# Kernel tuning notes

Hardware: AMD Instinct MI355X
Metric: run time of the kernel (lower is better)

Reference implementation:

```python
import jax, jax.numpy as jnp
import numpy as np

NU, NP, H = 100000, 200000, 128
EV, EL = 500000, 150000


def _sage(x_src, x_dst, src, dst, Wl, bl, Wr, n_dst):
    # PyG SAGEConv: lin_l(mean_j x_j) + lin_r(x_i); lin_l has bias, lin_r does not.
    msg = x_src[src]                                             # [E, H] gather
    agg = jax.ops.segment_sum(msg, dst, num_segments=n_dst)      # [n_dst, H]
    cnt = jax.ops.segment_sum(jnp.ones((src.shape[0],), x_src.dtype), dst,
                              num_segments=n_dst)                # [n_dst]
    mean = agg / jnp.maximum(cnt, 1.0)[:, None]
    return mean @ Wl.T + bl + x_dst @ Wr.T


def _hetero_layer(xu, xp, Wl, bl, Wr, ev_s, ev_d, el_s, el_d):
    # relation order: 0 viewed(u->p), 1 rev_viewed(p->u), 2 liked(u->p), 3 rev_liked(p->u)
    post = (_sage(xu, xp, ev_s, ev_d, Wl[0], bl[0], Wr[0], NP)
            + _sage(xu, xp, el_s, el_d, Wl[2], bl[2], Wr[2], NP))
    user = (_sage(xp, xu, ev_d, ev_s, Wl[1], bl[1], Wr[1], NU)
            + _sage(xp, xu, el_d, el_s, Wl[3], bl[3], Wr[3], NU))
    return user, post


def setup_inputs() -> dict:
    key = jax.random.key(0)
    ks = jax.random.split(key, 9)
    s = 1.0 / np.sqrt(H)
    return {
        "emb_user": jax.random.normal(ks[0], (NU, H), jnp.float32),
        "emb_post": jax.random.normal(ks[1], (NP, H), jnp.float32),
        "W_l": jax.random.normal(ks[2], (2, 4, H, H), jnp.float32) * s,
        "b_l": jnp.zeros((2, 4, H), jnp.float32),
        "W_r": jax.random.normal(ks[3], (2, 4, H, H), jnp.float32) * s,
        "viewed_src": jax.random.randint(ks[4], (EV,), 0, NU, jnp.int32),
        "viewed_dst": jax.random.randint(ks[5], (EV,), 0, NP, jnp.int32),
        "liked_src": jax.random.randint(ks[6], (EL,), 0, NU, jnp.int32),
        "liked_dst": jax.random.randint(ks[7], (EL,), 0, NP, jnp.int32),
    }


def reference(emb_user, emb_post, W_l, b_l, W_r,
              viewed_src, viewed_dst, liked_src, liked_dst):
    xu, xp = _hetero_layer(emb_user, emb_post, W_l[0], b_l[0], W_r[0],
                           viewed_src, viewed_dst, liked_src, liked_dst)
    xu, xp = jax.nn.relu(xu), jax.nn.relu(xp)
    xu, xp = _hetero_layer(xu, xp, W_l[1], b_l[1], W_r[1],
                           viewed_src, viewed_dst, liked_src, liked_dst)
    return xu, xp
```

## Files before the change

kernel.cpp:

```cpp
#include <hip/hip_runtime.h>
#include <hip/hip_bf16.h>

#define H 128

using bf16x8  = __attribute__((ext_vector_type(8))) short;
using floatx4 = __attribute__((ext_vector_type(4))) float;

static __device__ __forceinline__ short f2bf(float f) {
  union { float f; unsigned u; } v; v.f = f;
  unsigned r = v.u + 0x7fffu + ((v.u >> 16) & 1u);
  return (short)(r >> 16);
}
static __device__ __forceinline__ float bf2f(short s) {
  union { unsigned u; float f; } v; v.u = ((unsigned)(unsigned short)s) << 16;
  return v.f;
}

__global__ void count_edges2(const int* __restrict__ ev_s, const int* __restrict__ ev_d, int EV,
                             const int* __restrict__ el_s, const int* __restrict__ el_d, int EL,
                             int* __restrict__ cnt, int oV_u, int oV_p, int oL_u, int oL_p) {
  int i = blockIdx.x * blockDim.x + threadIdx.x;
  if (i < EV) {
    atomicAdd(&cnt[oV_u + ev_s[i]], 1);
    atomicAdd(&cnt[oV_p + ev_d[i]], 1);
  } else if (i - EV < EL) {
    int e = i - EV;
    atomicAdd(&cnt[oL_u + el_s[e]], 1);
    atomicAdd(&cnt[oL_p + el_d[e]], 1);
  }
}

__global__ __launch_bounds__(256) void scan_k1(const int* __restrict__ cnt, int* __restrict__ off,
                                               int* __restrict__ bsums, int4 starts, int4 lens) {
  int a = blockIdx.y;
  int start = ((const int*)&starts)[a];
  int len   = ((const int*)&lens)[a];
  int chunk = blockIdx.x * 1024;
  if (chunk >= len) return;
  const int* in = cnt + start;
  int* out = off + start;
  int tid = threadIdx.x;
  int base = chunk + tid * 4;
  int v[4];
#pragma unroll
  for (int j = 0; j < 4; ++j) v[j] = (base + j < len) ? in[base + j] : 0;
  int s = v[0] + v[1] + v[2] + v[3];
  __shared__ int lds[256];
  lds[tid] = s; __syncthreads();
  for (int o = 1; o < 256; o <<= 1) {
    int t = (tid >= o) ? lds[tid - o] : 0;
    __syncthreads();
    lds[tid] += t;
    __syncthreads();
  }
  int run = lds[tid] - s;
#pragma unroll
  for (int j = 0; j < 4; ++j) { if (base + j < len) out[base + j] = run; run += v[j]; }
  if (tid == 255) bsums[a * 256 + blockIdx.x] = lds[255];
}

__global__ __launch_bounds__(256) void scan_k2(int* __restrict__ bsums, int4 lens) {
  int a = blockIdx.x;
  int len = ((const int*)&lens)[a];
  int nb = (len + 1023) >> 10;
  int tid = threadIdx.x;
  int s = (tid < nb) ? bsums[a * 256 + tid] : 0;
  __shared__ int lds[256];
  lds[tid] = s; __syncthreads();
  for (int o = 1; o < 256; o <<= 1) {
    int t = (tid >= o) ? lds[tid - o] : 0;
    __syncthreads();
    lds[tid] += t;
    __syncthreads();
  }
  bsums[a * 256 + tid] = lds[tid] - s;
}

__global__ __launch_bounds__(256) void scan_k3(int* __restrict__ off, const int* __restrict__ bsums,
                                               int4 starts, int4 lens) {
  int a = blockIdx.y;
  int start = ((const int*)&starts)[a];
  int len   = ((const int*)&lens)[a];
  int chunk = blockIdx.x * 1024;
  if (chunk >= len) return;
  int add = bsums[a * 256 + blockIdx.x];
  int* out = off + start;
  int base = chunk + threadIdx.x * 4;
#pragma unroll
  for (int j = 0; j < 4; ++j) if (base + j < len) out[base + j] += add;
}

__global__ void fill_csr2(const int* __restrict__ ev_s, const int* __restrict__ ev_d, int EV,
                          const int* __restrict__ el_s, const int* __restrict__ el_d, int EL,
                          const int* __restrict__ off, int* __restrict__ cur,
                          int* __restrict__ sV_p, int* __restrict__ sV_u,
                          int* __restrict__ sL_p, int* __restrict__ sL_u,
                          int oV_p, int oV_u, int oL_p, int oL_u) {
  int i = blockIdx.x * blockDim.x + threadIdx.x;
  if (i < EV) {
    int s = ev_s[i], d = ev_d[i];
    sV_p[off[oV_p + d] + atomicAdd(&cur[oV_p + d], 1)] = s;
    sV_u[off[oV_u + s] + atomicAdd(&cur[oV_u + s], 1)] = d;
  } else if (i - EV < EL) {
    int e = i - EV;
    int s = el_s[e], d = el_d[e];
    sL_p[off[oL_p + d] + atomicAdd(&cur[oL_p + d], 1)] = s;
    sL_u[off[oL_u + s] + atomicAdd(&cur[oL_u + s], 1)] = d;
  }
}

__global__ void cvt_bf16_2(const float* __restrict__ inU, short* __restrict__ outU, int nU,
                           const float* __restrict__ inP, short* __restrict__ outP, int nP) {
  int idx = (blockIdx.x * blockDim.x + threadIdx.x) * 4;
  const float* in; short* out;
  if (idx < nU) { in = inU + idx; out = outU + idx; }
  else {
    idx -= nU;
    if (idx >= nP) return;
    in = inP + idx; out = outP + idx;
  }
  float4 v = *(const float4*)in;
  short4 o = { f2bf(v.x), f2bf(v.y), f2bf(v.z), f2bf(v.w) };
  *(short4*)out = o;
}

static __device__ __forceinline__ int wswz(int e) {
  int n = e >> 7, k = e & 127;
  int jt = n >> 4, r = n & 15;
  int kk = k >> 5, q = (k >> 3) & 3, j = k & 7;
  return (((jt * 4 + kk) * 64 + q * 16 + r) << 3) + j;
}
__global__ void prep_weights(const float* __restrict__ W_l, const float* __restrict__ b_l,
                             const float* __restrict__ W_r,
                             short* __restrict__ Wbf, float* __restrict__ bc) {
  int i = blockIdx.x * blockDim.x + threadIdx.x;
  if (i >= 4 * 16384) return;
  int s = i >> 14, e = i & 16383;
  int l = s >> 1, t = s & 1;
  int rA = t ? 1 : 0, rB = t ? 3 : 2;
  const float* WA = W_l + ((size_t)(l * 4 + rA) << 14);
  const float* WB = W_l + ((size_t)(l * 4 + rB) << 14);
  const float* RA = W_r + ((size_t)(l * 4 + rA) << 14);
  const float* RB = W_r + ((size_t)(l * 4 + rB) << 14);
  short* o = Wbf + (size_t)s * 3 * 16384;
  int d = wswz(e);
  o[d]             = f2bf(WA[e]);
  o[16384 + d]     = f2bf(WB[e]);
  o[2 * 16384 + d] = f2bf(RA[e] + RB[e]);
  if (e < H) bc[s * H + e] = b_l[(l * 4 + rA) * H + e] + b_l[(l * 4 + rB) * H + e];
}

__global__ __launch_bounds__(256) void aggregate2(
    const bf16x8* __restrict__ xA,
    const int* __restrict__ sVA, const int* __restrict__ oVA, const int* __restrict__ cVA,
    const int* __restrict__ sLA, const int* __restrict__ oLA, const int* __restrict__ cLA,
    bf16x8* __restrict__ mVA, bf16x8* __restrict__ mLA, int NA, int nbA,
    const bf16x8* __restrict__ xB,
    const int* __restrict__ sVB, const int* __restrict__ oVB, const int* __restrict__ cVB,
    const int* __restrict__ sLB, const int* __restrict__ oLB, const int* __restrict__ cLB,
    bf16x8* __restrict__ mVB, bf16x8* __restrict__ mLB, int NB) {
  int b = blockIdx.x;
  const bf16x8* x; const int *sV, *oV, *cV, *sL, *oL, *cL;
  bf16x8 *mV, *mL; int N, t0;
  if (b < nbA) {
    x = xA; sV = sVA; oV = oVA; cV = cVA; sL = sLA; oL = oLA; cL = cLA;
    mV = mVA; mL = mLA; N = NA; t0 = b * 256;
  } else {
    x = xB; sV = sVB; oV = oVB; cV = cVB; sL = sLB; oL = oLB; cL = cLB;
    mV = mVB; mL = mLB; N = NB; t0 = (b - nbA) * 256;
  }
  int t = t0 + threadIdx.x;
  int node = t >> 4, c = t & 15;
  if (node >= N) return;

  int oVn = oV[node], nV = cV[node];
  int oLn = oL[node], nL = cL[node];

  bf16x8 pAL{}, pBL{};
  if (nL > 0) pAL = x[(size_t)sL[oLn] * 16 + c];
  if (nL > 1) pBL = x[(size_t)sL[oLn + 1] * 16 + c];

  float acc[8];
  {
#pragma unroll
    for (int j = 0; j < 8; ++j) acc[j] = 0.f;
    int i = 0;
    for (; i + 4 <= nV; i += 4) {
      int s0 = sV[oVn + i], s1 = sV[oVn + i + 1], s2 = sV[oVn + i + 2], s3 = sV[oVn + i + 3];
      bf16x8 v0 = x[(size_t)s0 * 16 + c];
      bf16x8 v1 = x[(size_t)s1 * 16 + c];
      bf16x8 v2 = x[(size_t)s2 * 16 + c];
      bf16x8 v3 = x[(size_t)s3 * 16 + c];
#pragma unroll
      for (int j = 0; j < 8; ++j) acc[j] += bf2f(v0[j]);
#pragma unroll
      for (int j = 0; j < 8; ++j) acc[j] += bf2f(v1[j]);
#pragma unroll
      for (int j = 0; j < 8; ++j) acc[j] += bf2f(v2[j]);
#pragma unroll
      for (int j = 0; j < 8; ++j) acc[j] += bf2f(v3[j]);
    }
    for (; i < nV; ++i) {
      bf16x8 v = x[(size_t)sV[oVn + i] * 16 + c];
#pragma unroll
      for (int j = 0; j < 8; ++j) acc[j] += bf2f(v[j]);
    }
    float rin = 1.0f / fmaxf((float)nV, 1.0f);
    bf16x8 w;
#pragma unroll
    for (int j = 0; j < 8; ++j) w[j] = f2bf(acc[j] * rin);
    mV[(size_t)node * 16 + c] = w;
  }
  {
#pragma unroll
    for (int j = 0; j < 8; ++j) acc[j] = 0.f;
    if (nL > 0) {
#pragma unroll
      for (int j = 0; j < 8; ++j) acc[j] += bf2f(pAL[j]);
    }
    if (nL > 1) {
#pragma unroll
      for (int j = 0; j < 8; ++j) acc[j] += bf2f(pBL[j]);
    }
    int i = 2;
    for (; i + 4 <= nL; i += 4) {
      int s0 = sL[oLn + i], s1 = sL[oLn + i + 1], s2 = sL[oLn + i + 2], s3 = sL[oLn + i + 3];
      bf16x8 v0 = x[(size_t)s0 * 16 + c];
      bf16x8 v1 = x[(size_t)s1 * 16 + c];
      bf16x8 v2 = x[(size_t)s2 * 16 + c];
      bf16x8 v3 = x[(size_t)s3 * 16 + c];
#pragma unroll
      for (int j = 0; j < 8; ++j) acc[j] += bf2f(v0[j]);
#pragma unroll
      for (int j = 0; j < 8; ++j) acc[j] += bf2f(v1[j]);
#pragma unroll
      for (int j = 0; j < 8; ++j) acc[j] += bf2f(v2[j]);
#pragma unroll
      for (int j = 0; j < 8; ++j) acc[j] += bf2f(v3[j]);
    }
    for (; i < nL; ++i) {
      bf16x8 v = x[(size_t)sL[oLn + i] * 16 + c];
#pragma unroll
      for (int j = 0; j < 8; ++j) acc[j] += bf2f(v[j]);
    }
    float rin = 1.0f / fmaxf((float)nL, 1.0f);
    bf16x8 w;
#pragma unroll
    for (int j = 0; j < 8; ++j) w[j] = f2bf(acc[j] * rin);
    mL[(size_t)node * 16 + c] = w;
  }
}

__global__ __launch_bounds__(512, 1) void fused_gemm2(
    const short* __restrict__ mVA, const short* __restrict__ mLA, const short* __restrict__ xbA,
    const short* __restrict__ WAp, const float* __restrict__ biasA,
    float* __restrict__ o32A, short* __restrict__ o16A, int NA, int nbA,
    const short* __restrict__ mVB, const short* __restrict__ mLB, const short* __restrict__ xbB,
    const short* __restrict__ WBp, const float* __restrict__ biasB,
    float* __restrict__ o32B, short* __restrict__ o16B, int NB, int relu) {
  extern __shared__ short Wlds[];
  int b = blockIdx.x;
  const short *mV, *mL, *xb, *W; const float* bias;
  float* out32; short* out16; int N, nbPart, bLoc;
  if (b < nbA) {
    mV = mVA; mL = mLA; xb = xbA; W = WAp; bias = biasA;
    out32 = o32A; out16 = o16A; N = NA; nbPart = nbA; bLoc = b;
  } else {
    mV = mVB; mL = mLB; xb = xbB; W = WBp; bias = biasB;
    out32 = o32B; out16 = o16B; N = NB; nbPart = gridDim.x - nbA; bLoc = b - nbA;
  }

  int tid = threadIdx.x;
#pragma unroll
  for (int it = 0; it < 12; ++it) {
    int c = it * 512 + tid;
    *(bf16x8*)(Wlds + (size_t)c * 8) = *(const bf16x8*)(W + (size_t)c * 8);
  }
  __syncthreads();

  int wave = tid >> 6, lane = tid & 63;
  int r = lane & 15, quad = lane >> 4;

  float bias_r[8];
#pragma unroll
  for (int jt = 0; jt < 8; ++jt) bias_r[jt] = bias[jt * 16 + r];

  int nrgTot = (N + 31) >> 5;
  int wStride = nbPart * 8;
  int wBase = bLoc * 8 + wave;
  int nrgW = (wBase < nrgTot) ? (nrgTot - wBase + wStride - 1) / wStride : 0;

  floatx4 acc[2][8];
#pragma unroll
  for (int t = 0; t < 2; ++t)
#pragma unroll
    for (int j = 0; j < 8; ++j) acc[t][j] = floatx4{0.f, 0.f, 0.f, 0.f};

  auto issueA = [&](int j, int m, bf16x8 (&buf)[2][4]) {
    if (j >= nrgW) return;
    int rowb = (wBase + j * wStride) << 5;
    const short* X = (m == 0) ? mV : (m == 1) ? mL : xb;
#pragma unroll
    for (int t = 0; t < 2; ++t) {
      int row = rowb + t * 16 + r;
      row = row < N ? row : N - 1;
      const short* Xr = X + (size_t)row * H + quad * 8;
#pragma unroll
      for (int kk = 0; kk < 4; ++kk) buf[t][kk] = *(const bf16x8*)(Xr + kk * 32);
    }
  };

  auto computeB = [&](int m, bf16x8 (&buf)[2][4]) {
    const short* Wm = Wlds + m * 16384;
#pragma unroll
    for (int kk = 0; kk < 4; ++kk) {
#pragma unroll
      for (int jt = 0; jt < 8; ++jt) {
        bf16x8 bfR = *(const bf16x8*)(Wm + (size_t)((jt * 4 + kk) * 64 + lane) * 8);
        acc[0][jt] = __builtin_amdgcn_mfma_f32_16x16x32_bf16(buf[0][kk], bfR, acc[0][jt], 0, 0, 0);
        acc[1][jt] = __builtin_amdgcn_mfma_f32_16x16x32_bf16(buf[1][kk], bfR, acc[1][jt], 0, 0, 0);
      }
    }
  };

  auto epi = [&](int j) {
    int rowb = (wBase + j * wStride) << 5;
#pragma unroll
    for (int t = 0; t < 2; ++t) {
#pragma unroll
      for (int jt = 0; jt < 8; ++jt) {
        int ocol = jt * 16 + r;
        float bv = bias_r[jt];
#pragma unroll
        for (int g = 0; g < 4; ++g) {
          int orow = rowb + t * 16 + quad * 4 + g;
          if (orow < N) {
            float v = acc[t][jt][g] + bv;
            if (relu) v = fmaxf(v, 0.f);
            if (out32) out32[(size_t)orow * H + ocol] = v;
            else       out16[(size_t)orow * H + ocol] = f2bf(v);
          }
        }
        acc[t][jt] = floatx4{0.f, 0.f, 0.f, 0.f};
      }
    }
  };

  bf16x8 A0[2][4], A1[2][4], A2[2][4];
  issueA(0, 0, A0);
  issueA(0, 1, A1);
  for (int j = 0; j < nrgW; ++j) {
    issueA(j, 2, A2);
    computeB(0, A0);
    issueA(j + 1, 0, A0);
    computeB(1, A1);
    issueA(j + 1, 1, A1);
    computeB(2, A2);
    epi(j);
  }
}

extern "C" void kernel_launch(void* const* d_in, const int* in_sizes, int n_in,
                              void* d_out, int out_size, void* d_ws, size_t ws_size,
                              hipStream_t stream) {
  const float* emb_user = (const float*)d_in[0];
  const float* emb_post = (const float*)d_in[1];
  const float* W_l = (const float*)d_in[2];
  const float* b_l = (const float*)d_in[3];
  const float* W_r = (const float*)d_in[4];
  const int* ev_s = (const int*)d_in[5];
  const int* ev_d = (const int*)d_in[6];
  const int* el_s = (const int*)d_in[7];
  const int* el_d = (const int*)d_in[8];

  const int NU = in_sizes[0] / H;
  const int NP = in_sizes[1] / H;
  const int EV = in_sizes[5];
  const int EL = in_sizes[7];
  const int T = 2 * NP + 2 * NU;
  const size_t NUH = (size_t)NU * H, NPH = (size_t)NP * H;

  char* p = (char*)d_ws;
  auto alloc = [&](size_t bytes) -> void* {
    void* q = (void*)p; p += (bytes + 255) & ~(size_t)255; return q;
  };
  int*   cnt   = (int*)alloc((size_t)T * 4);
  int*   cur   = (int*)alloc((size_t)T * 4);
  int*   off   = (int*)alloc((size_t)T * 4);
  int*   bsums = (int*)alloc(4 * 256 * 4);
  int*   sV_p  = (int*)alloc((size_t)EV * 4);
  int*   sV_u  = (int*)alloc((size_t)EV * 4);
  int*   sL_p  = (int*)alloc((size_t)EL * 4);
  int*   sL_u  = (int*)alloc((size_t)EL * 4);
  short* Wbf   = (short*)alloc((size_t)4 * 3 * 16384 * 2);
  float* bc    = (float*)alloc(4 * H * 4);
  short* xbf_u  = (short*)alloc(NUH * 2);
  short* xbf_p  = (short*)alloc(NPH * 2);
  short* xbf1_u = (short*)alloc(NUH * 2);
  short* xbf1_p = (short*)alloc(NPH * 2);
  short* mVp    = (short*)alloc(NPH * 2);
  short* mLp    = (short*)alloc(NPH * 2);
  short* mVu    = (short*)alloc(NUH * 2);
  short* mLu    = (short*)alloc(NUH * 2);

  float* out_u_final = (float*)d_out;
  float* out_p_final = (float*)d_out + NUH;

  const int oV_p = 0, oL_p = NP, oV_u = 2 * NP, oL_u = 2 * NP + NU;

  hipMemsetAsync(cnt, 0, (size_t)T * 4, stream);
  hipMemsetAsync(cur, 0, (size_t)T * 4, stream);
  count_edges2<<<(EV + EL + 255) / 256, 256, 0, stream>>>(
      ev_s, ev_d, EV, el_s, el_d, EL, cnt, oV_u, oV_p, oL_u, oL_p);

  int4 starts = { oV_p, oL_p, oV_u, oL_u };
  int4 lens   = { NP, NP, NU, NU };
  int maxb = ((NP > NU ? NP : NU) + 1023) / 1024;
  dim3 gscan(maxb, 4, 1);
  scan_k1<<<gscan, 256, 0, stream>>>(cnt, off, bsums, starts, lens);
  scan_k2<<<4, 256, 0, stream>>>(bsums, lens);
  scan_k3<<<gscan, 256, 0, stream>>>(off, bsums, starts, lens);

  fill_csr2<<<(EV + EL + 255) / 256, 256, 0, stream>>>(
      ev_s, ev_d, EV, el_s, el_d, EL, off, cur,
      sV_p, sV_u, sL_p, sL_u, oV_p, oV_u, oL_p, oL_u);

  cvt_bf16_2<<<((int)((NUH + NPH) / 4) + 255) / 256, 256, 0, stream>>>(
      emb_user, xbf_u, (int)NUH, emb_post, xbf_p, (int)NPH);
  prep_weights<<<(4 * 16384 + 255) / 256, 256, 0, stream>>>(W_l, b_l, W_r, Wbf, bc);

  const int ldsBytes = 3 * 16384 * 2;
  hipFuncSetAttribute((const void*)fused_gemm2, hipFuncAttributeMaxDynamicSharedMemorySize,
                      ldsBytes);

  int nbAggP = (NP + 15) / 16;
  int nbAggU = (NU + 15) / 16;

  const int GB = 256;
  int nbP = (int)(((long long)GB * NP) / ((long long)NP + NU));
  if (nbP < 1) nbP = 1;
  if (nbP > GB - 1) nbP = GB - 1;

  for (int l = 0; l < 2; ++l) {
    const short* xu = l ? xbf1_u : xbf_u;
    const short* xp = l ? xbf1_p : xbf_p;
    const short* Wpost = Wbf + (size_t)(l * 2 + 0) * 3 * 16384;
    const short* Wuser = Wbf + (size_t)(l * 2 + 1) * 3 * 16384;
    const float* bpost = bc + (l * 2 + 0) * H;
    const float* buser = bc + (l * 2 + 1) * H;

    aggregate2<<<nbAggP + nbAggU, 256, 0, stream>>>(
        (const bf16x8*)xu,
        sV_p, off + oV_p, cnt + oV_p,
        sL_p, off + oL_p, cnt + oL_p,
        (bf16x8*)mVp, (bf16x8*)mLp, NP, nbAggP,
        (const bf16x8*)xp,
        sV_u, off + oV_u, cnt + oV_u,
        sL_u, off + oL_u, cnt + oL_u,
        (bf16x8*)mVu, (bf16x8*)mLu, NU);

    fused_gemm2<<<GB, 512, ldsBytes, stream>>>(
        mVp, mLp, xp, Wpost, bpost,
        l ? out_p_final : nullptr, l ? nullptr : xbf1_p, NP, nbP,
        mVu, mLu, xu, Wuser, buser,
        l ? out_u_final : nullptr, l ? nullptr : xbf1_u, NU, l == 0);
  }
}
```

Before: 730.6 us.

## Fuse preprocessing kernels and record edge slots during counting to drop second atomics

The edge-count, bf16 embedding conversion and weight-prep kernels are merged into one launch. The counting pass now saves each edge's atomicAdd return value as its slot. The CSR fill uses those stored slots instead of a second round of atomics on a separate cursor array, which also removes one memset. In exchange, four slot arrays must be written and then read back.

```diff
diff --git a/kernel.cpp b/kernel.cpp
--- a/kernel.cpp
+++ b/kernel.cpp
@@ -16,19 +16,17 @@
   return v.f;
 }
 
-__global__ void count_edges2(const int* __restrict__ ev_s, const int* __restrict__ ev_d, int EV,
-                             const int* __restrict__ el_s, const int* __restrict__ el_d, int EL,
-                             int* __restrict__ cnt, int oV_u, int oV_p, int oL_u, int oL_p) {
-  int i = blockIdx.x * blockDim.x + threadIdx.x;
-  if (i < EV) {
-    atomicAdd(&cnt[oV_u + ev_s[i]], 1);
-    atomicAdd(&cnt[oV_p + ev_d[i]], 1);
-  } else if (i - EV < EL) {
-    int e = i - EV;
-    atomicAdd(&cnt[oL_u + el_s[e]], 1);
-    atomicAdd(&cnt[oL_p + el_d[e]], 1);
-  }
-}
+__global__ __launch_bounds__(256) void preproc_a(
+    const int* __restrict__ ev_s, const int* __restrict__ ev_d, int EV,
+    const int* __restrict__ el_s, const int* __restrict__ el_d, int EL,
+    int* __restrict__ cnt, int oV_u, int oV_p, int oL_u, int oL_p,
+    int* __restrict__ slotVp, int* __restrict__ slotVu,
+    int* __restrict__ slotLp, int* __restrict__ slotLu,
+    const float* __restrict__ embU, short* __restrict__ xbfU, int nU,
+    const float* __restrict__ embP, short* __restrict__ xbfP, int nP,
+    const float* __restrict__ W_l, const float* __restrict__ b_l,
+    const float* __restrict__ W_r,
+    short* __restrict__ Wbf, float* __restrict__ bc, int nbCnt, int nbCvt);
 
 __global__ __launch_bounds__(256) void scan_k1(const int* __restrict__ cnt, int* __restrict__ off,
                                                int* __restrict__ bsums, int4 starts, int4 lens) {
@@ -90,64 +88,83 @@
   for (int j = 0; j < 4; ++j) if (base + j < len) out[base + j] += add;
 }
 
-__global__ void fill_csr2(const int* __restrict__ ev_s, const int* __restrict__ ev_d, int EV,
+__global__ __launch_bounds__(256) void preproc_a(
+    const int* __restrict__ ev_s, const int* __restrict__ ev_d, int EV,
+    const int* __restrict__ el_s, const int* __restrict__ el_d, int EL,
+    int* __restrict__ cnt, int oV_u, int oV_p, int oL_u, int oL_p,
+    int* __restrict__ slotVp, int* __restrict__ slotVu,
+    int* __restrict__ slotLp, int* __restrict__ slotLu,
+    const float* __restrict__ embU, short* __restrict__ xbfU, int nU,
+    const float* __restrict__ embP, short* __restrict__ xbfP, int nP,
+    const float* __restrict__ W_l, const float* __restrict__ b_l,
+    const float* __restrict__ W_r,
+    short* __restrict__ Wbf, float* __restrict__ bc, int nbCnt, int nbCvt) {
+  int b = blockIdx.x;
+  if (b < nbCnt) {
+    int i = b * 256 + threadIdx.x;
+    if (i < EV) {
+      int s = ev_s[i], d = ev_d[i];
+      slotVu[i] = atomicAdd(&cnt[oV_u + s], 1);
+      slotVp[i] = atomicAdd(&cnt[oV_p + d], 1);
+    } else if (i - EV < EL) {
+      int e = i - EV;
+      int s = el_s[e], d = el_d[e];
+      slotLu[e] = atomicAdd(&cnt[oL_u + s], 1);
+      slotLp[e] = atomicAdd(&cnt[oL_p + d], 1);
+    }
+  } else if (b < nbCnt + nbCvt) {
+    int idx = ((b - nbCnt) * 256 + threadIdx.x) * 4;
+    const float* in; short* out;
+    if (idx < nU) { in = embU + idx; out = xbfU + idx; }
+    else {
+      idx -= nU;
+      if (idx >= nP) return;
+      in = embP + idx; out = xbfP + idx;
+    }
+    float4 v = *(const float4*)in;
+    short4 o = { f2bf(v.x), f2bf(v.y), f2bf(v.z), f2bf(v.w) };
+    *(short4*)out = o;
+  } else {
+    int i = (b - nbCnt - nbCvt) * 256 + threadIdx.x;
+    if (i >= 4 * 16384) return;
+    int s = i >> 14, e = i & 16383;
+    int l = s >> 1, t = s & 1;
+    int rA = t ? 1 : 0, rB = t ? 3 : 2;
+    const float* WA = W_l + ((size_t)(l * 4 + rA) << 14);
+    const float* WB = W_l + ((size_t)(l * 4 + rB) << 14);
+    const float* RA = W_r + ((size_t)(l * 4 + rA) << 14);
+    const float* RB = W_r + ((size_t)(l * 4 + rB) << 14);
+    short* o = Wbf + (size_t)s * 3 * 16384;
+    int n = e >> 7, k = e & 127;
+    int jt = n >> 4, r = n & 15;
+    int kk = k >> 5, q = (k >> 3) & 3, j = k & 7;
+    int d = (((jt * 4 + kk) * 64 + q * 16 + r) << 3) + j;
+    o[d]             = f2bf(WA[e]);
+    o[16384 + d]     = f2bf(WB[e]);
+    o[2 * 16384 + d] = f2bf(RA[e] + RB[e]);
+    if (e < H) bc[s * H + e] = b_l[(l * 4 + rA) * H + e] + b_l[(l * 4 + rB) * H + e];
+  }
+}
+
+__global__ void fill_csr3(const int* __restrict__ ev_s, const int* __restrict__ ev_d, int EV,
                           const int* __restrict__ el_s, const int* __restrict__ el_d, int EL,
-                          const int* __restrict__ off, int* __restrict__ cur,
+                          const int* __restrict__ off,
+                          const int* __restrict__ slotVp, const int* __restrict__ slotVu,
+                          const int* __restrict__ slotLp, const int* __restrict__ slotLu,
                           int* __restrict__ sV_p, int* __restrict__ sV_u,
                           int* __restrict__ sL_p, int* __restrict__ sL_u,
                           int oV_p, int oV_u, int oL_p, int oL_u) {
   int i = blockIdx.x * blockDim.x + threadIdx.x;
   if (i < EV) {
     int s = ev_s[i], d = ev_d[i];
-    sV_p[off[oV_p + d] + atomicAdd(&cur[oV_p + d], 1)] = s;
-    sV_u[off[oV_u + s] + atomicAdd(&cur[oV_u + s], 1)] = d;
+    sV_p[off[oV_p + d] + slotVp[i]] = s;
+    sV_u[off[oV_u + s] + slotVu[i]] = d;
   } else if (i - EV < EL) {
     int e = i - EV;
     int s = el_s[e], d = el_d[e];
-    sL_p[off[oL_p + d] + atomicAdd(&cur[oL_p + d], 1)] = s;
-    sL_u[off[oL_u + s] + atomicAdd(&cur[oL_u + s], 1)] = d;
-  }
-}
-
-__global__ void cvt_bf16_2(const float* __restrict__ inU, short* __restrict__ outU, int nU,
-                           const float* __restrict__ inP, short* __restrict__ outP, int nP) {
-  int idx = (blockIdx.x * blockDim.x + threadIdx.x) * 4;
-  const float* in; short* out;
-  if (idx < nU) { in = inU + idx; out = outU + idx; }
-  else {
-    idx -= nU;
-    if (idx >= nP) return;
-    in = inP + idx; out = outP + idx;
-  }
-  float4 v = *(const float4*)in;
-  short4 o = { f2bf(v.x), f2bf(v.y), f2bf(v.z), f2bf(v.w) };
-  *(short4*)out = o;
-}
-
-static __device__ __forceinline__ int wswz(int e) {
-  int n = e >> 7, k = e & 127;
-  int jt = n >> 4, r = n & 15;
-  int kk = k >> 5, q = (k >> 3) & 3, j = k & 7;
-  return (((jt * 4 + kk) * 64 + q * 16 + r) << 3) + j;
-}
-__global__ void prep_weights(const float* __restrict__ W_l, const float* __restrict__ b_l,
-                             const float* __restrict__ W_r,
-                             short* __restrict__ Wbf, float* __restrict__ bc) {
-  int i = blockIdx.x * blockDim.x + threadIdx.x;
-  if (i >= 4 * 16384) return;
-  int s = i >> 14, e = i & 16383;
-  int l = s >> 1, t = s & 1;
-  int rA = t ? 1 : 0, rB = t ? 3 : 2;
-  const float* WA = W_l + ((size_t)(l * 4 + rA) << 14);
-  const float* WB = W_l + ((size_t)(l * 4 + rB) << 14);
-  const float* RA = W_r + ((size_t)(l * 4 + rA) << 14);
-  const float* RB = W_r + ((size_t)(l * 4 + rB) << 14);
-  short* o = Wbf + (size_t)s * 3 * 16384;
-  int d = wswz(e);
-  o[d]             = f2bf(WA[e]);
-  o[16384 + d]     = f2bf(WB[e]);
-  o[2 * 16384 + d] = f2bf(RA[e] + RB[e]);
-  if (e < H) bc[s * H + e] = b_l[(l * 4 + rA) * H + e] + b_l[(l * 4 + rB) * H + e];
+    sL_p[off[oL_p + d] + slotLp[e]] = s;
+    sL_u[off[oL_u + s] + slotLu[e]] = d;
+  }
 }
 
 __global__ __launch_bounds__(256) void aggregate2(
@@ -385,9 +402,12 @@
     void* q = (void*)p; p += (bytes + 255) & ~(size_t)255; return q;
   };
   int*   cnt   = (int*)alloc((size_t)T * 4);
-  int*   cur   = (int*)alloc((size_t)T * 4);
   int*   off   = (int*)alloc((size_t)T * 4);
   int*   bsums = (int*)alloc(4 * 256 * 4);
+  int*   slotVp = (int*)alloc((size_t)EV * 4);
+  int*   slotVu = (int*)alloc((size_t)EV * 4);
+  int*   slotLp = (int*)alloc((size_t)EL * 4);
+  int*   slotLu = (int*)alloc((size_t)EL * 4);
   int*   sV_p  = (int*)alloc((size_t)EV * 4);
   int*   sV_u  = (int*)alloc((size_t)EV * 4);
   int*   sL_p  = (int*)alloc((size_t)EL * 4);
@@ -409,9 +429,16 @@
   const int oV_p = 0, oL_p = NP, oV_u = 2 * NP, oL_u = 2 * NP + NU;
 
   hipMemsetAsync(cnt, 0, (size_t)T * 4, stream);
-  hipMemsetAsync(cur, 0, (size_t)T * 4, stream);
-  count_edges2<<<(EV + EL + 255) / 256, 256, 0, stream>>>(
-      ev_s, ev_d, EV, el_s, el_d, EL, cnt, oV_u, oV_p, oL_u, oL_p);
+
+  int nbCnt = (EV + EL + 255) / 256;
+  int nbCvt = ((int)((NUH + NPH) / 4) + 255) / 256;
+  int nbPrep = (4 * 16384 + 255) / 256;
+  preproc_a<<<nbCnt + nbCvt + nbPrep, 256, 0, stream>>>(
+      ev_s, ev_d, EV, el_s, el_d, EL,
+      cnt, oV_u, oV_p, oL_u, oL_p,
+      slotVp, slotVu, slotLp, slotLu,
+      emb_user, xbf_u, (int)NUH, emb_post, xbf_p, (int)NPH,
+      W_l, b_l, W_r, Wbf, bc, nbCnt, nbCvt);
 
   int4 starts = { oV_p, oL_p, oV_u, oL_u };
   int4 lens   = { NP, NP, NU, NU };
@@ -421,13 +448,10 @@
   scan_k2<<<4, 256, 0, stream>>>(bsums, lens);
   scan_k3<<<gscan, 256, 0, stream>>>(off, bsums, starts, lens);
 
-  fill_csr2<<<(EV + EL + 255) / 256, 256, 0, stream>>>(
-      ev_s, ev_d, EV, el_s, el_d, EL, off, cur,
+  fill_csr3<<<(EV + EL + 255) / 256, 256, 0, stream>>>(
+      ev_s, ev_d, EV, el_s, el_d, EL, off,
+      slotVp, slotVu, slotLp, slotLu,
       sV_p, sV_u, sL_p, sL_u, oV_p, oV_u, oL_p, oL_u);
-
-  cvt_bf16_2<<<((int)((NUH + NPH) / 4) + 255) / 256, 256, 0, stream>>>(
-      emb_user, xbf_u, (int)NUH, emb_post, xbf_p, (int)NPH);
-  prep_weights<<<(4 * 16384 + 255) / 256, 256, 0, stream>>>(W_l, b_l, W_r, Wbf, bc);
 
   const int ldsBytes = 3 * 16384 * 2;
   hipFuncSetAttribute((const void*)fused_gemm2, hipFuncAttributeMaxDynamicSharedMemorySize,
```

After: 665.3 us. -8.9%, faster.
